# Optimization experiments

Measured on AMD Instinct MI355X. Metric: run time of the kernel, lower is better.

## Reference

```python
import jax, jax.numpy as jnp
import numpy as np


def gcn_conv(x, row, col, W, b, n_nodes):
    """PyG GCNConv: x' = D^-1/2 (A+I) D^-1/2 (x W) + b, with self-loops in row/col."""
    xw = x @ W  # [N, out]
    deg = jax.ops.segment_sum(jnp.ones_like(col, dtype=xw.dtype), col, num_segments=n_nodes)
    d_inv_sqrt = jnp.where(deg > 0, jax.lax.rsqrt(deg), 0.0)
    norm = d_inv_sqrt[row] * d_inv_sqrt[col]  # [E+N]
    msgs = norm[:, None] * xw[row]            # gather + scale
    out = jax.ops.segment_sum(msgs, col, num_segments=n_nodes)  # scatter-add to dst
    return out + b


def setup_inputs() -> dict:
    key = jax.random.key(0)
    ks = jax.random.split(key, 8)
    N, E = 100000, 1600000
    d_in, d_h, d_out = 128, 128, 64
    x = jax.random.normal(ks[0], (N, d_in), dtype=jnp.float32)
    edge_index = jax.random.randint(ks[1], (2, E), 0, N, dtype=jnp.int32)
    s = 1.0 / np.sqrt(d_in)
    W1 = jax.random.uniform(ks[2], (d_in, d_h), jnp.float32, -s, s)
    b1 = jnp.zeros((d_h,), jnp.float32)
    sh = 1.0 / np.sqrt(d_h)
    W2 = jax.random.uniform(ks[3], (d_h, d_h), jnp.float32, -sh, sh)
    b2 = jnp.zeros((d_h,), jnp.float32)
    W3 = jax.random.uniform(ks[4], (d_h, d_out), jnp.float32, -sh, sh)
    b3 = jnp.zeros((d_out,), jnp.float32)
    return {"x": x, "edge_index": edge_index, "W1": W1, "b1": b1,
            "W2": W2, "b2": b2, "W3": W3, "b3": b3}


def reference(x, edge_index, W1, b1, W2, b2, W3, b3):
    n_nodes = x.shape[0]
    loops = jnp.arange(n_nodes, dtype=edge_index.dtype)
    row = jnp.concatenate([edge_index[0], loops])  # src (with self-loops)
    col = jnp.concatenate([edge_index[1], loops])  # dst (with self-loops)
    # dropout p=0.0 / eval mode -> identity, omitted
    h = jax.nn.relu(gcn_conv(x, row, col, W1, b1, n_nodes))
    h = jax.nn.relu(gcn_conv(h, row, col, W2, b2, n_nodes))
    out = gcn_conv(h, row, col, W3, b3, n_nodes)
    return out
```

## Files before the change

### kernel.cpp

```cpp
#include <hip/hip_runtime.h>
#include <hip/hip_fp16.h>

typedef _Float16 half8 __attribute__((ext_vector_type(8)));
typedef float floatx4 __attribute__((ext_vector_type(4)));

#define NCH 128
#define TILE 2048
#define CSLOT 48
#define MAXNB 1024
#define MAXCH 1024
#define OVFCAP 65536
#define AGG_GRID 2048

__global__ __launch_bounds__(256) void part_k(const int* __restrict__ row,
                                              const int* __restrict__ col, int E,
                                              int chunk, int NB,
                                              int* __restrict__ stg_d,
                                              int* __restrict__ stg_s,
                                              int* __restrict__ cnts,
                                              unsigned long long* __restrict__ ovf,
                                              int* __restrict__ ovfcnt,
                                              const float* __restrict__ W1,
                                              const float* __restrict__ W2,
                                              const float* __restrict__ W3,
                                              __half* __restrict__ Wt1,
                                              __half* __restrict__ Wt2,
                                              __half* __restrict__ Wt3) {
    __shared__ int bd[NCH][CSLOT];
    __shared__ int bs[NCH][CSLOT];
    __shared__ int lcnt[NCH];
    __shared__ int lpref[NCH + 1];
    int tid = threadIdx.x;
    int b = blockIdx.x;

    int idx = b * 256 + tid;
    if (idx < 16384) {
        int k = idx >> 7, nn = idx & 127;
        Wt1[nn * 128 + k] = __float2half(W1[idx]);
    } else if (idx < 32768) {
        int j = idx - 16384;
        int k = j >> 7, nn = j & 127;
        Wt2[nn * 128 + k] = __float2half(W2[j]);
    } else if (idx < 40960) {
        int j = idx - 32768;
        int k = j >> 6, nn = j & 63;
        Wt3[nn * 128 + k] = __float2half(W3[j]);
    }

    for (int i = tid; i < NCH; i += 256) lcnt[i] = 0;
    __syncthreads();

    int i0 = b * TILE + tid * 8;
    int sv[8], dv[8];
    int nv = 0;
    if (i0 + 7 < E && (E & 3) == 0) {
        int4 r0 = *(const int4*)(row + i0);
        int4 r1 = *(const int4*)(row + i0 + 4);
        int4 c0 = *(const int4*)(col + i0);
        int4 c1 = *(const int4*)(col + i0 + 4);
        sv[0] = r0.x; sv[1] = r0.y; sv[2] = r0.z; sv[3] = r0.w;
        sv[4] = r1.x; sv[5] = r1.y; sv[6] = r1.z; sv[7] = r1.w;
        dv[0] = c0.x; dv[1] = c0.y; dv[2] = c0.z; dv[3] = c0.w;
        dv[4] = c1.x; dv[5] = c1.y; dv[6] = c1.z; dv[7] = c1.w;
        nv = 8;
    } else {
#pragma unroll
        for (int j = 0; j < 8; j++) {
            if (i0 + j < E) { sv[nv] = row[i0 + j]; dv[nv] = col[i0 + j]; nv++; }
        }
    }
#pragma unroll 8
    for (int j = 0; j < nv; j++) {
        int d = dv[j], s = sv[j];
        int c = d / chunk;
        int r = atomicAdd(&lcnt[c], 1);
        if (r < CSLOT) {
            bd[c][r] = d;
            bs[c][r] = s;
        } else {
            int o = atomicAdd(ovfcnt, 1);
            if (o < OVFCAP)
                ovf[o] = ((unsigned long long)(unsigned)d << 32) | (unsigned)s;
        }
    }
    __syncthreads();
    if (tid == 0) {
        int a = 0;
#pragma unroll
        for (int c = 0; c < NCH; c++) {
            lpref[c] = a;
            a += min(lcnt[c], CSLOT);
        }
        lpref[NCH] = a;
    }
    __syncthreads();
    for (int c = tid; c < NCH; c += 256) cnts[(size_t)c * NB + b] = min(lcnt[c], CSLOT);
    int total = lpref[NCH];
    for (int f = tid; f < total; f += 256) {
        int lo = 0, hi = NCH;
        while (hi - lo > 1) {
            int mid = (lo + hi) >> 1;
            if (lpref[mid] <= f) lo = mid; else hi = mid;
        }
        int slot = f - lpref[lo];
        size_t cell = ((size_t)lo * NB + b) * CSLOT;
        stg_d[cell + slot] = bd[lo][slot];
        stg_s[cell + slot] = bs[lo][slot];
    }
}

__global__ __launch_bounds__(512) void csr_hist_k(const int* __restrict__ stg_d,
                                                  const int* __restrict__ cnts, int NB,
                                                  int N, int chunk,
                                                  const unsigned long long* __restrict__ ovf,
                                                  const int* __restrict__ ovfcnt,
                                                  int* __restrict__ deg,
                                                  float* __restrict__ dinv,
                                                  int* __restrict__ csum) {
    __shared__ int hist[MAXCH];
    __shared__ int red[512];
    int c = blockIdx.x, tid = threadIdx.x;
    int dlo = c * chunk;
    int dhi = min(N, dlo + chunk);
    int csz = dhi - dlo;
    if (csz <= 0) {
        if (tid == 0) csum[c] = 0;
        return;
    }
    for (int i = tid; i < csz; i += 512) hist[i] = 1;
    __syncthreads();
    for (int b0 = tid >> 4; b0 < NB; b0 += 32) {
        int cnt = cnts[(size_t)c * NB + b0];
        size_t base = ((size_t)c * NB + b0) * CSLOT;
        for (int slot = tid & 15; slot < cnt; slot += 16)
            atomicAdd(&hist[stg_d[base + slot] - dlo], 1);
    }
    int oc = min(*ovfcnt, OVFCAP);
    for (int i = tid; i < oc; i += 512) {
        int d = (int)(ovf[i] >> 32);
        if (d >= dlo && d < dhi) atomicAdd(&hist[d - dlo], 1);
    }
    __syncthreads();
    int t = 0;
    for (int i = tid; i < csz; i += 512) {
        int dg = hist[i];
        deg[dlo + i] = dg;
        dinv[dlo + i] = rsqrtf((float)dg);
        t += dg;
    }
    red[tid] = t;
    __syncthreads();
    for (int o = 256; o > 0; o >>= 1) {
        if (tid < o) red[tid] += red[tid + o];
        __syncthreads();
    }
    if (tid == 0) csum[c] = red[0];
}

__global__ __launch_bounds__(512) void csr_fill_k(const int* __restrict__ stg_d,
                                                  const int* __restrict__ stg_s,
                                                  const int* __restrict__ cnts, int NB,
                                                  const int* __restrict__ deg,
                                                  const int* __restrict__ csum,
                                                  int N, int chunk,
                                                  const unsigned long long* __restrict__ ovf,
                                                  const int* __restrict__ ovfcnt,
                                                  int* __restrict__ cptr,
                                                  int* __restrict__ meta) {
    __shared__ int cur[MAXCH];
    __shared__ int sc[512];
    int c = blockIdx.x, tid = threadIdx.x;
    int dlo = c * chunk;
    int dhi = min(N, dlo + chunk);
    int csz = dhi - dlo;
    if (csz <= 0) return;

    sc[tid] = (tid < NCH && tid < c) ? csum[tid] : 0;
    __syncthreads();
    for (int o = 256; o > 0; o >>= 1) {
        if (tid < o) sc[tid] += sc[tid + o];
        __syncthreads();
    }
    int cbase = sc[0];
    __syncthreads();

    int i0 = tid * 2;
    int v0 = (i0 < csz) ? deg[dlo + i0] : 0;
    int v1 = (i0 + 1 < csz) ? deg[dlo + i0 + 1] : 0;
    int s = v0 + v1;
    sc[tid] = s;
    __syncthreads();
    for (int o = 1; o < 512; o <<= 1) {
        int tmp = 0;
        if (tid >= o) tmp = sc[tid - o];
        __syncthreads();
        sc[tid] += tmp;
        __syncthreads();
    }
    int off = cbase + sc[tid] - s;
    if (i0 < csz) {
        cur[i0] = off;
        cptr[dlo + i0] = off;
        off += v0;
        if (i0 + 1 < csz) {
            cur[i0 + 1] = off;
            cptr[dlo + i0 + 1] = off;
        }
    }
    if (dhi == N && tid == 511) cptr[N] = cbase + sc[511];
    __syncthreads();

    for (int b0 = tid >> 4; b0 < NB; b0 += 32) {
        int cnt = cnts[(size_t)c * NB + b0];
        size_t base = ((size_t)c * NB + b0) * CSLOT;
        for (int slot = tid & 15; slot < cnt; slot += 16) {
            int d = stg_d[base + slot];
            int sv = stg_s[base + slot];
            int p = atomicAdd(&cur[d - dlo], 1);
            meta[p] = sv;
        }
    }
    for (int i = tid; i < csz; i += 512) {
        int p = atomicAdd(&cur[i], 1);
        meta[p] = dlo + i;
    }
    int oc = min(*ovfcnt, OVFCAP);
    for (int i = tid; i < oc; i += 512) {
        unsigned long long v = ovf[i];
        int d = (int)(v >> 32);
        if (d >= dlo && d < dhi) {
            int p = atomicAdd(&cur[d - dlo], 1);
            meta[p] = (int)(v & 0xffffffffull);
        }
    }
}

template <typename AT, int DOUT>
__global__ __launch_bounds__(256) void gemm_mfma(const AT* __restrict__ A,
                                                 const __half* __restrict__ Wt,
                                                 const float* __restrict__ dinv,
                                                 __half* __restrict__ C, int n) {
    constexpr int CT = DOUT / 16;
    constexpr int WP = 136;
    __shared__ _Float16 ldsW[DOUT * WP];
    int tid = threadIdx.x;
    int lane = tid & 63;
    int wid = tid >> 6;
    for (int i = tid; i < DOUT * 16; i += 256) {
        int nrow = i >> 4;
        int kc = (i & 15) * 8;
        *(half8*)(&ldsW[nrow * WP + kc]) =
            *(const half8*)((const _Float16*)Wt + nrow * 128 + kc);
    }
    __syncthreads();
    int rwb = blockIdx.x * 128 + wid * 32;
    int m = lane & 15;
    int quad = lane >> 4;
    floatx4 acc[2][CT];
#pragma unroll
    for (int t = 0; t < 2; t++)
#pragma unroll
        for (int c = 0; c < CT; c++) acc[t][c] = (floatx4){0.f, 0.f, 0.f, 0.f};

#pragma unroll
    for (int kq = 0; kq < 4; kq++) {
        int k0 = kq * 32 + quad * 8;
        half8 afr[2];
#pragma unroll
        for (int t = 0; t < 2; t++) {
            int r = rwb + t * 16 + m;
            r = r < n ? r : n - 1;
            const AT* ap = A + (size_t)r * 128 + k0;
            if constexpr (sizeof(AT) == 2) {
                afr[t] = *(const half8*)ap;
            } else {
                float4 f0 = *(const float4*)ap;
                float4 f1 = *(const float4*)(ap + 4);
                half8 h;
                h[0] = (_Float16)f0.x; h[1] = (_Float16)f0.y;
                h[2] = (_Float16)f0.z; h[3] = (_Float16)f0.w;
                h[4] = (_Float16)f1.x; h[5] = (_Float16)f1.y;
                h[6] = (_Float16)f1.z; h[7] = (_Float16)f1.w;
                afr[t] = h;
            }
        }
#pragma unroll
        for (int c = 0; c < CT; c++) {
            half8 bfr = *(const half8*)(&ldsW[(c * 16 + m) * WP + k0]);
#pragma unroll
            for (int t = 0; t < 2; t++)
                acc[t][c] =
                    __builtin_amdgcn_mfma_f32_16x16x32_f16(afr[t], bfr, acc[t][c], 0, 0, 0);
        }
    }
#pragma unroll
    for (int t = 0; t < 2; t++) {
#pragma unroll
        for (int reg = 0; reg < 4; reg++) {
            int r = rwb + t * 16 + quad * 4 + reg;
            if (r < n) {
                float dv = dinv[r];
#pragma unroll
                for (int c = 0; c < CT; c++)
                    C[(size_t)r * DOUT + c * 16 + m] = __float2half(acc[t][c][reg] * dv);
            }
        }
    }
    if (blockIdx.x == 0 && tid < DOUT / 8) {
        half8 z = (half8){0, 0, 0, 0, 0, 0, 0, 0};
        *(half8*)((_Float16*)C + (size_t)n * DOUT + tid * 8) = z;
    }
}

template <int D, bool RELU, typename OT>
__global__ __launch_bounds__(256) void aggregate_k(const __half* __restrict__ xw,
                                                   const int* __restrict__ ptr,
                                                   const int* __restrict__ meta,
                                                   const float* __restrict__ bias,
                                                   const float* __restrict__ dinv,
                                                   OT* __restrict__ out, int n) {
    constexpr int GS = D / 8;
    constexpr int EPW = 64 / GS;
    constexpr int UNR = 4;
    __shared__ int smeta[4][64];
    int lane = threadIdx.x & 63;
    int wid = threadIdx.x >> 6;
    int sub = lane / GS;
    int cg = lane % GS;
    const _Float16* xp = (const _Float16*)xw + cg * 8;

    for (int node = blockIdx.x * 4 + wid; node < n; node += gridDim.x * 4) {
        int e0 = ptr[node], e1 = ptr[node + 1];
        float dv = dinv[node];
        float acc[8];
#pragma unroll
        for (int i = 0; i < 8; i++) acc[i] = 0.f;

        for (int base = e0; base < e1; base += 64) {
            int cnt = min(e1 - base, 64);
            if (lane < cnt) smeta[wid][lane] = meta[base + lane];
            for (int j = 0; j < cnt; j += UNR * EPW) {
                int sreg[UNR];
#pragma unroll
                for (int u = 0; u < UNR; u++) {
                    int e = j + u * EPW + sub;
                    e = (e < 64) ? e : 0;
                    int t = smeta[wid][e];
                    sreg[u] = (j + u * EPW + sub < cnt) ? t : n;
                }
                half8 vreg[UNR];
#pragma unroll
                for (int u = 0; u < UNR; u++)
                    vreg[u] = *(const half8*)(xp + (size_t)sreg[u] * D);
#pragma unroll
                for (int u = 0; u < UNR; u++)
#pragma unroll
                    for (int i = 0; i < 8; i++)
                        acc[i] += (float)vreg[u][i];
            }
        }
#pragma unroll
        for (int off = GS; off < 64; off <<= 1) {
#pragma unroll
            for (int i = 0; i < 8; i++) acc[i] += __shfl_xor(acc[i], off, 64);
        }
        if (lane < GS) {
            float4 bb0 = *(const float4*)(bias + cg * 8);
            float4 bb1 = *(const float4*)(bias + cg * 8 + 4);
            float r[8];
            r[0] = acc[0] * dv + bb0.x; r[1] = acc[1] * dv + bb0.y;
            r[2] = acc[2] * dv + bb0.z; r[3] = acc[3] * dv + bb0.w;
            r[4] = acc[4] * dv + bb1.x; r[5] = acc[5] * dv + bb1.y;
            r[6] = acc[6] * dv + bb1.z; r[7] = acc[7] * dv + bb1.w;
            if (RELU) {
#pragma unroll
                for (int i = 0; i < 8; i++) r[i] = fmaxf(r[i], 0.f);
            }
            if constexpr (sizeof(OT) == 2) {
                half8 h;
#pragma unroll
                for (int i = 0; i < 8; i++) h[i] = (_Float16)r[i];
                *(half8*)((_Float16*)out + (size_t)node * D + cg * 8) = h;
            } else {
                float* op = (float*)out + (size_t)node * D + cg * 8;
                *(float4*)op = make_float4(r[0], r[1], r[2], r[3]);
                *(float4*)(op + 4) = make_float4(r[4], r[5], r[6], r[7]);
            }
        }
    }
}

extern "C" void kernel_launch(void* const* d_in, const int* in_sizes, int n_in,
                              void* d_out, int out_size, void* d_ws, size_t ws_size,
                              hipStream_t stream) {
    const float* x = (const float*)d_in[0];
    const int* ei = (const int*)d_in[1];
    const float* W1 = (const float*)d_in[2];
    const float* b1 = (const float*)d_in[3];
    const float* W2 = (const float*)d_in[4];
    const float* b2 = (const float*)d_in[5];
    const float* W3 = (const float*)d_in[6];
    const float* b3 = (const float*)d_in[7];
    float* out = (float*)d_out;
    int N = in_sizes[0] / 128;
    int E = in_sizes[1] / 2;
    const int* row = ei;
    const int* col = ei + E;
    int T = E + N;

    char* w = (char*)d_ws;
    size_t off = 0;
    auto alloc = [&](size_t bytes) -> void* {
        void* p = w + off;
        off = (off + bytes + 511) & ~(size_t)511;
        return p;
    };
    __half* bufH = (__half*)alloc((size_t)(N + 1) * 128 * 2);
    __half* bufA = (__half*)alloc((size_t)N * 128 * 2);
    __half* Wt1 = (__half*)alloc(16384 * 2);
    __half* Wt2 = (__half*)alloc(16384 * 2);
    __half* Wt3 = (__half*)alloc(8192 * 2);
    int* deg = (int*)alloc((size_t)N * 4);
    float* dinv = (float*)alloc((size_t)N * 4);
    int* cptr = (int*)alloc((size_t)(N + 1) * 4);
    int* meta = (int*)alloc((size_t)T * 4);
    int* csum = (int*)alloc(NCH * 4);
    int* ovfcnt = (int*)alloc(64);
    unsigned long long* ovf = (unsigned long long*)alloc((size_t)OVFCAP * 8);
    int NB = (E + TILE - 1) / TILE;
    int* cnts = (int*)alloc((size_t)NCH * NB * 4);
    int chunk = (N + NCH - 1) / NCH;

    int* stg_d = (int*)bufH;
    int* stg_s = (int*)bufA;

    hipMemsetAsync(ovfcnt, 0, 4, stream);
    part_k<<<NB, 256, 0, stream>>>(row, col, E, chunk, NB, stg_d, stg_s, cnts, ovf, ovfcnt,
                                   W1, W2, W3, Wt1, Wt2, Wt3);
    csr_hist_k<<<NCH, 512, 0, stream>>>(stg_d, cnts, NB, N, chunk, ovf, ovfcnt, deg, dinv, csum);
    csr_fill_k<<<NCH, 512, 0, stream>>>(stg_d, stg_s, cnts, NB, deg, csum, N, chunk, ovf,
                                        ovfcnt, cptr, meta);

    int gb = (N + 127) / 128;
    gemm_mfma<float, 128><<<gb, 256, 0, stream>>>(x, Wt1, dinv, bufH, N);
    aggregate_k<128, true, __half><<<AGG_GRID, 256, 0, stream>>>(bufH, cptr, meta, b1, dinv, bufA, N);
    gemm_mfma<__half, 128><<<gb, 256, 0, stream>>>(bufA, Wt2, dinv, bufH, N);
    aggregate_k<128, true, __half><<<AGG_GRID, 256, 0, stream>>>(bufH, cptr, meta, b2, dinv, bufA, N);
    gemm_mfma<__half, 64><<<gb, 256, 0, stream>>>(bufA, Wt3, dinv, bufH, N);
    aggregate_k<64, false, float><<<AGG_GRID, 256, 0, stream>>>(bufH, cptr, meta, b3, dinv, out, N);
}
```

Measured before the change: 371.7 us.

## Merge CSR histogram and fill kernels, pack edge pairs, cache chunk edges in LDS

Packs each (dst,src) edge into one 64-bit staging entry, so each edge needs a single store and load instead of two. Per-chunk totals are accumulated with atomics in the partition kernel. The separate histogram and fill kernels become one kernel that builds degrees, offsets and dinv, and buffers the chunk's edges in shared memory for the fill pass. This removes one launch and the second global read of staged edges. The cost is a large LDS footprint (about 120KB) that limits occupancy, and a slower fallback path when a chunk overflows the buffer.

```diff
diff --git a/kernel.cpp b/kernel.cpp
--- a/kernel.cpp
+++ b/kernel.cpp
@@ -3,22 +3,23 @@
 
 typedef _Float16 half8 __attribute__((ext_vector_type(8)));
 typedef float floatx4 __attribute__((ext_vector_type(4)));
+typedef unsigned long long u64;
 
 #define NCH 128
 #define TILE 2048
 #define CSLOT 48
-#define MAXNB 1024
-#define MAXCH 1024
+#define MAXCH2 800
+#define PLCAP 14336
 #define OVFCAP 65536
 #define AGG_GRID 2048
 
 __global__ __launch_bounds__(256) void part_k(const int* __restrict__ row,
                                               const int* __restrict__ col, int E,
                                               int chunk, int NB,
-                                              int* __restrict__ stg_d,
-                                              int* __restrict__ stg_s,
+                                              u64* __restrict__ stg_p,
                                               int* __restrict__ cnts,
-                                              unsigned long long* __restrict__ ovf,
+                                              int* __restrict__ chunkTot,
+                                              u64* __restrict__ ovf,
                                               int* __restrict__ ovfcnt,
                                               const float* __restrict__ W1,
                                               const float* __restrict__ W2,
@@ -26,8 +27,7 @@
                                               __half* __restrict__ Wt1,
                                               __half* __restrict__ Wt2,
                                               __half* __restrict__ Wt3) {
-    __shared__ int bd[NCH][CSLOT];
-    __shared__ int bs[NCH][CSLOT];
+    __shared__ u64 bkt[NCH][CSLOT];
     __shared__ int lcnt[NCH];
     __shared__ int lpref[NCH + 1];
     int tid = threadIdx.x;
@@ -74,14 +74,20 @@
         int d = dv[j], s = sv[j];
         int c = d / chunk;
         int r = atomicAdd(&lcnt[c], 1);
+        u64 pair = ((u64)(unsigned)d << 32) | (unsigned)s;
         if (r < CSLOT) {
-            bd[c][r] = d;
-            bs[c][r] = s;
+            bkt[c][r] = pair;
         } else {
             int o = atomicAdd(ovfcnt, 1);
-            if (o < OVFCAP)
-                ovf[o] = ((unsigned long long)(unsigned)d << 32) | (unsigned)s;
-        }
+            if (o < OVFCAP) ovf[o] = pair;
+        }
+    }
+    __syncthreads();
+    if (tid < NCH) {
+        int cc = min(lcnt[tid], CSLOT);
+        lcnt[tid] = cc;
+        cnts[(size_t)tid * NB + b] = cc;
+        atomicAdd(&chunkTot[tid * 16], cc);
     }
     __syncthreads();
     if (tid == 0) {
@@ -89,12 +95,11 @@
 #pragma unroll
         for (int c = 0; c < NCH; c++) {
             lpref[c] = a;
-            a += min(lcnt[c], CSLOT);
+            a += lcnt[c];
         }
         lpref[NCH] = a;
     }
     __syncthreads();
-    for (int c = tid; c < NCH; c += 256) cnts[(size_t)c * NB + b] = min(lcnt[c], CSLOT);
     int total = lpref[NCH];
     for (int f = tid; f < total; f += 256) {
         int lo = 0, hi = NCH;
@@ -103,90 +108,67 @@
             if (lpref[mid] <= f) lo = mid; else hi = mid;
         }
         int slot = f - lpref[lo];
-        size_t cell = ((size_t)lo * NB + b) * CSLOT;
-        stg_d[cell + slot] = bd[lo][slot];
-        stg_s[cell + slot] = bs[lo][slot];
+        stg_p[((size_t)lo * NB + b) * CSLOT + slot] = bkt[lo][slot];
     }
 }
 
-__global__ __launch_bounds__(512) void csr_hist_k(const int* __restrict__ stg_d,
-                                                  const int* __restrict__ cnts, int NB,
-                                                  int N, int chunk,
-                                                  const unsigned long long* __restrict__ ovf,
-                                                  const int* __restrict__ ovfcnt,
-                                                  int* __restrict__ deg,
-                                                  float* __restrict__ dinv,
-                                                  int* __restrict__ csum) {
-    __shared__ int hist[MAXCH];
-    __shared__ int red[512];
-    int c = blockIdx.x, tid = threadIdx.x;
-    int dlo = c * chunk;
-    int dhi = min(N, dlo + chunk);
-    int csz = dhi - dlo;
-    if (csz <= 0) {
-        if (tid == 0) csum[c] = 0;
-        return;
-    }
-    for (int i = tid; i < csz; i += 512) hist[i] = 1;
-    __syncthreads();
-    for (int b0 = tid >> 4; b0 < NB; b0 += 32) {
-        int cnt = cnts[(size_t)c * NB + b0];
-        size_t base = ((size_t)c * NB + b0) * CSLOT;
-        for (int slot = tid & 15; slot < cnt; slot += 16)
-            atomicAdd(&hist[stg_d[base + slot] - dlo], 1);
-    }
-    int oc = min(*ovfcnt, OVFCAP);
-    for (int i = tid; i < oc; i += 512) {
-        int d = (int)(ovf[i] >> 32);
-        if (d >= dlo && d < dhi) atomicAdd(&hist[d - dlo], 1);
-    }
-    __syncthreads();
-    int t = 0;
-    for (int i = tid; i < csz; i += 512) {
-        int dg = hist[i];
-        deg[dlo + i] = dg;
-        dinv[dlo + i] = rsqrtf((float)dg);
-        t += dg;
-    }
-    red[tid] = t;
-    __syncthreads();
-    for (int o = 256; o > 0; o >>= 1) {
-        if (tid < o) red[tid] += red[tid + o];
-        __syncthreads();
-    }
-    if (tid == 0) csum[c] = red[0];
-}
-
-__global__ __launch_bounds__(512) void csr_fill_k(const int* __restrict__ stg_d,
-                                                  const int* __restrict__ stg_s,
-                                                  const int* __restrict__ cnts, int NB,
-                                                  const int* __restrict__ deg,
-                                                  const int* __restrict__ csum,
-                                                  int N, int chunk,
-                                                  const unsigned long long* __restrict__ ovf,
-                                                  const int* __restrict__ ovfcnt,
-                                                  int* __restrict__ cptr,
-                                                  int* __restrict__ meta) {
-    __shared__ int cur[MAXCH];
+__global__ __launch_bounds__(512) void csr_build_k(const u64* __restrict__ stg_p,
+                                                   const int* __restrict__ cnts,
+                                                   const int* __restrict__ chunkTot,
+                                                   int NB, int N, int chunk,
+                                                   const u64* __restrict__ ovf,
+                                                   const int* __restrict__ ovfcnt,
+                                                   float* __restrict__ dinv,
+                                                   int* __restrict__ cptr,
+                                                   int* __restrict__ meta) {
+    __shared__ int hist[MAXCH2];
+    __shared__ int cur[MAXCH2];
     __shared__ int sc[512];
+    __shared__ u64 pl[PLCAP];
+    __shared__ int plcnt;
     int c = blockIdx.x, tid = threadIdx.x;
     int dlo = c * chunk;
     int dhi = min(N, dlo + chunk);
     int csz = dhi - dlo;
     if (csz <= 0) return;
-
-    sc[tid] = (tid < NCH && tid < c) ? csum[tid] : 0;
+    if (tid == 0) plcnt = 0;
+    for (int i = tid; i < csz; i += 512) hist[i] = 1;
+
+    int part = 0;
+    for (int i = tid; i < c; i += 512) part += chunkTot[i * 16];
+    int oc = min(*ovfcnt, OVFCAP);
+    for (int i = tid; i < oc; i += 512) {
+        int d = (int)(ovf[i] >> 32);
+        if (d < dlo) part++;
+    }
+    sc[tid] = part;
     __syncthreads();
     for (int o = 256; o > 0; o >>= 1) {
         if (tid < o) sc[tid] += sc[tid + o];
         __syncthreads();
     }
-    int cbase = sc[0];
+    int cbase = dlo + sc[0];
+    __syncthreads();
+
+    for (int b0 = tid >> 4; b0 < NB; b0 += 32) {
+        int cnt = cnts[(size_t)c * NB + b0];
+        size_t base = ((size_t)c * NB + b0) * CSLOT;
+        for (int slot = tid & 15; slot < cnt; slot += 16) {
+            u64 v = stg_p[base + slot];
+            atomicAdd(&hist[(int)(v >> 32) - dlo], 1);
+            int p = atomicAdd(&plcnt, 1);
+            if (p < PLCAP) pl[p] = v;
+        }
+    }
+    for (int i = tid; i < oc; i += 512) {
+        int d = (int)(ovf[i] >> 32);
+        if (d >= dlo && d < dhi) atomicAdd(&hist[d - dlo], 1);
+    }
     __syncthreads();
 
     int i0 = tid * 2;
-    int v0 = (i0 < csz) ? deg[dlo + i0] : 0;
-    int v1 = (i0 + 1 < csz) ? deg[dlo + i0 + 1] : 0;
+    int v0 = (i0 < csz) ? hist[i0] : 0;
+    int v1 = (i0 + 1 < csz) ? hist[i0 + 1] : 0;
     int s = v0 + v1;
     sc[tid] = s;
     __syncthreads();
@@ -201,36 +183,45 @@
     if (i0 < csz) {
         cur[i0] = off;
         cptr[dlo + i0] = off;
+        dinv[dlo + i0] = rsqrtf((float)v0);
         off += v0;
         if (i0 + 1 < csz) {
             cur[i0 + 1] = off;
             cptr[dlo + i0 + 1] = off;
+            dinv[dlo + i0 + 1] = rsqrtf((float)v1);
         }
     }
     if (dhi == N && tid == 511) cptr[N] = cbase + sc[511];
     __syncthreads();
 
-    for (int b0 = tid >> 4; b0 < NB; b0 += 32) {
-        int cnt = cnts[(size_t)c * NB + b0];
-        size_t base = ((size_t)c * NB + b0) * CSLOT;
-        for (int slot = tid & 15; slot < cnt; slot += 16) {
-            int d = stg_d[base + slot];
-            int sv = stg_s[base + slot];
-            int p = atomicAdd(&cur[d - dlo], 1);
-            meta[p] = sv;
+    int pc = plcnt;
+    if (pc <= PLCAP) {
+        for (int i = tid; i < pc; i += 512) {
+            u64 v = pl[i];
+            int p = atomicAdd(&cur[(int)(v >> 32) - dlo], 1);
+            meta[p] = (int)(v & 0xffffffffULL);
+        }
+    } else {
+        for (int b0 = tid >> 4; b0 < NB; b0 += 32) {
+            int cnt = cnts[(size_t)c * NB + b0];
+            size_t base = ((size_t)c * NB + b0) * CSLOT;
+            for (int slot = tid & 15; slot < cnt; slot += 16) {
+                u64 v = stg_p[base + slot];
+                int p = atomicAdd(&cur[(int)(v >> 32) - dlo], 1);
+                meta[p] = (int)(v & 0xffffffffULL);
+            }
         }
     }
     for (int i = tid; i < csz; i += 512) {
         int p = atomicAdd(&cur[i], 1);
         meta[p] = dlo + i;
     }
-    int oc = min(*ovfcnt, OVFCAP);
     for (int i = tid; i < oc; i += 512) {
-        unsigned long long v = ovf[i];
+        u64 v = ovf[i];
         int d = (int)(v >> 32);
         if (d >= dlo && d < dhi) {
             int p = atomicAdd(&cur[d - dlo], 1);
-            meta[p] = (int)(v & 0xffffffffull);
+            meta[p] = (int)(v & 0xffffffffULL);
         }
     }
 }
@@ -344,9 +335,8 @@
 #pragma unroll
                 for (int u = 0; u < UNR; u++) {
                     int e = j + u * EPW + sub;
-                    e = (e < 64) ? e : 0;
                     int t = smeta[wid][e];
-                    sreg[u] = (j + u * EPW + sub < cnt) ? t : n;
+                    sreg[u] = (e < cnt) ? t : n;
                 }
                 half8 vreg[UNR];
 #pragma unroll
@@ -420,26 +410,25 @@
     __half* Wt1 = (__half*)alloc(16384 * 2);
     __half* Wt2 = (__half*)alloc(16384 * 2);
     __half* Wt3 = (__half*)alloc(8192 * 2);
-    int* deg = (int*)alloc((size_t)N * 4);
     float* dinv = (float*)alloc((size_t)N * 4);
     int* cptr = (int*)alloc((size_t)(N + 1) * 4);
     int* meta = (int*)alloc((size_t)T * 4);
-    int* csum = (int*)alloc(NCH * 4);
-    int* ovfcnt = (int*)alloc(64);
-    unsigned long long* ovf = (unsigned long long*)alloc((size_t)OVFCAP * 8);
+    int* ctblock = (int*)alloc(128 * 64 + 64);
+    u64* ovf = (u64*)alloc((size_t)OVFCAP * 8);
     int NB = (E + TILE - 1) / TILE;
     int* cnts = (int*)alloc((size_t)NCH * NB * 4);
     int chunk = (N + NCH - 1) / NCH;
 
-    int* stg_d = (int*)bufH;
-    int* stg_s = (int*)bufA;
-
-    hipMemsetAsync(ovfcnt, 0, 4, stream);
-    part_k<<<NB, 256, 0, stream>>>(row, col, E, chunk, NB, stg_d, stg_s, cnts, ovf, ovfcnt,
-                                   W1, W2, W3, Wt1, Wt2, Wt3);
-    csr_hist_k<<<NCH, 512, 0, stream>>>(stg_d, cnts, NB, N, chunk, ovf, ovfcnt, deg, dinv, csum);
-    csr_fill_k<<<NCH, 512, 0, stream>>>(stg_d, stg_s, cnts, NB, deg, csum, N, chunk, ovf,
-                                        ovfcnt, cptr, meta);
+    int* chunkTot = ctblock;
+    int* ovfcnt = ctblock + 2048;
+
+    u64* stg_p = (u64*)d_ws;
+
+    hipMemsetAsync(ctblock, 0, 128 * 64 + 64, stream);
+    part_k<<<NB, 256, 0, stream>>>(row, col, E, chunk, NB, stg_p, cnts, chunkTot,
+                                   ovf, ovfcnt, W1, W2, W3, Wt1, Wt2, Wt3);
+    csr_build_k<<<NCH, 512, 0, stream>>>(stg_p, cnts, chunkTot, NB, N, chunk, ovf,
+                                         ovfcnt, dinv, cptr, meta);
 
     int gb = (N + 127) / 128;
     gemm_mfma<float, 128><<<gb, 256, 0, stream>>>(x, Wt1, dinv, bufH, N);
```

Result: no change. 366.1 us (-1.5%).
